# Optimization experiments

Hardware: AMD Instinct MI355X
Metric: run time of the kernel (lower is better)

## Reference

```python
import jax, jax.numpy as jnp
import numpy as np

N_VARS = 1_000_000
N_CLAUSES = 4_000_000
CLAUSE_SIZE = 3


def setup_inputs() -> dict:
    key = jax.random.key(0)
    k1, k2, k3 = jax.random.split(key, 3)
    assignment_logits = jax.random.normal(k1, (N_VARS,), dtype=jnp.float32)
    vars_in_clause = jax.random.randint(k2, (N_CLAUSES, CLAUSE_SIZE), 0, N_VARS, dtype=jnp.int64)
    signs = jax.random.randint(k3, (N_CLAUSES, CLAUSE_SIZE), 0, 2, dtype=jnp.int64)
    return {"assignment_logits": assignment_logits, "vars_in_clause": vars_in_clause, "signs": signs}


def reference(assignment_logits, vars_in_clause, signs):
    # assignments: [n_variables] in (0,1)
    assignments = jax.nn.sigmoid(assignment_logits)
    # gather literal values per clause: [n_clauses, clause_size]
    gathered = assignments[vars_in_clause]
    literal_values = jnp.where(signs == 1, gathered, 1.0 - gathered)
    # per-clause max (soft OR), then global min (hard AND)
    clause_satisfactions = literal_values.max(axis=1)  # [n_clauses]
    all_satisfied = clause_satisfactions.min()
    n_satisfied = (clause_satisfactions > 0.5).astype(jnp.float32).sum()
    return assignments, clause_satisfactions, all_satisfied, n_satisfied
```

## Files before the change

kernel.cpp:

```cpp
#include <hip/hip_runtime.h>
#include <math.h>

#define NV 1000000
#define NC 4000000
#define NGROUP (NC / 4)
#define G2 (NGROUP / 2)
#define TPB 1024
#define TPB_A 256

typedef _Float16 half_t;
typedef _Float16 half4_t __attribute__((ext_vector_type(4)));
typedef int   vint4   __attribute__((ext_vector_type(4)));
typedef float vfloat4 __attribute__((ext_vector_type(4)));

__device__ __forceinline__ float sigf(float x) { return 1.0f / (1.0f + __expf(-x)); }

__global__ __launch_bounds__(TPB_A) void tbl_build(
    const float* __restrict__ logits,
    half_t* __restrict__ tbl,
    float* __restrict__ out)
{
    const int i = blockIdx.x * TPB_A + threadIdx.x;
    if (i == 0) {
        out[NV + NC]     = INFINITY;
        out[NV + NC + 1] = 0.0f;
    }
    if (i < NV / 4) {
        vfloat4 v = ((const vfloat4*)logits)[i];
        half4_t h;
        h.x = (half_t)sigf(v.x); h.y = (half_t)sigf(v.y);
        h.z = (half_t)sigf(v.z); h.w = (half_t)sigf(v.w);
        ((half4_t*)tbl)[i] = h;
    }
}

__device__ __forceinline__ float litv(float sg, int s) { return s ? sg : 1.0f - sg; }

__global__ __launch_bounds__(TPB) void sat_clauses(
    const float*  __restrict__ logits,
    const half_t* __restrict__ tbl,
    const vint4*  __restrict__ vars4,
    const vint4*  __restrict__ signs4,
    float* __restrict__ out)
{
    const int g = blockIdx.x * TPB + threadIdx.x;
    float minv = INFINITY;
    float fcnt = 0.0f;

    if (g < NV / 4) {
        vfloat4 v = ((const vfloat4*)logits)[g];
        vfloat4 r;
        r.x = sigf(v.x); r.y = sigf(v.y); r.z = sigf(v.z); r.w = sigf(v.w);
        ((vfloat4*)out)[g] = r;
    }

    if (g < G2) {
        const int h = g + G2;
        vint4 a0 = vars4[3 * g], a1 = vars4[3 * g + 1], a2 = vars4[3 * g + 2];
        vint4 b0 = vars4[3 * h], b1 = vars4[3 * h + 1], b2 = vars4[3 * h + 2];

        float u0  = (float)tbl[a0.x], u1  = (float)tbl[a0.y], u2  = (float)tbl[a0.z];
        float u3  = (float)tbl[a0.w], u4  = (float)tbl[a1.x], u5  = (float)tbl[a1.y];
        float u6  = (float)tbl[a1.z], u7  = (float)tbl[a1.w], u8  = (float)tbl[a2.x];
        float u9  = (float)tbl[a2.y], u10 = (float)tbl[a2.z], u11 = (float)tbl[a2.w];
        float w0  = (float)tbl[b0.x], w1  = (float)tbl[b0.y], w2  = (float)tbl[b0.z];
        float w3  = (float)tbl[b0.w], w4  = (float)tbl[b1.x], w5  = (float)tbl[b1.y];
        float w6  = (float)tbl[b1.z], w7  = (float)tbl[b1.w], w8  = (float)tbl[b2.x];
        float w9  = (float)tbl[b2.y], w10 = (float)tbl[b2.z], w11 = (float)tbl[b2.w];

        vint4 sa0 = signs4[3 * g], sa1 = signs4[3 * g + 1], sa2 = signs4[3 * g + 2];
        vint4 sb0 = signs4[3 * h], sb1 = signs4[3 * h + 1], sb2 = signs4[3 * h + 2];

        vfloat4 r, q;
        r.x = fmaxf(fmaxf(litv(u0, sa0.x), litv(u1,  sa0.y)), litv(u2,  sa0.z));
        r.y = fmaxf(fmaxf(litv(u3, sa0.w), litv(u4,  sa1.x)), litv(u5,  sa1.y));
        r.z = fmaxf(fmaxf(litv(u6, sa1.z), litv(u7,  sa1.w)), litv(u8,  sa2.x));
        r.w = fmaxf(fmaxf(litv(u9, sa2.y), litv(u10, sa2.z)), litv(u11, sa2.w));
        q.x = fmaxf(fmaxf(litv(w0, sb0.x), litv(w1,  sb0.y)), litv(w2,  sb0.z));
        q.y = fmaxf(fmaxf(litv(w3, sb0.w), litv(w4,  sb1.x)), litv(w5,  sb1.y));
        q.z = fmaxf(fmaxf(litv(w6, sb1.z), litv(w7,  sb1.w)), litv(w8,  sb2.x));
        q.w = fmaxf(fmaxf(litv(w9, sb2.y), litv(w10, sb2.z)), litv(w11, sb2.w));

        __builtin_nontemporal_store(r, (vfloat4*)(out + NV) + g);
        __builtin_nontemporal_store(q, (vfloat4*)(out + NV) + h);

        minv = fminf(fminf(fminf(r.x, r.y), fminf(r.z, r.w)),
                     fminf(fminf(q.x, q.y), fminf(q.z, q.w)));
        fcnt = (float)((r.x > 0.5f) + (r.y > 0.5f) + (r.z > 0.5f) + (r.w > 0.5f) +
                       (q.x > 0.5f) + (q.y > 0.5f) + (q.z > 0.5f) + (q.w > 0.5f));
    }

    #pragma unroll
    for (int off = 32; off > 0; off >>= 1) {
        minv = fminf(minv, __shfl_down(minv, off));
        fcnt += __shfl_down(fcnt, off);
    }
    __shared__ float smin[TPB / 64];
    __shared__ float scnt[TPB / 64];
    const int wave = threadIdx.x >> 6, lane = threadIdx.x & 63;
    if (lane == 0) { smin[wave] = minv; scnt[wave] = fcnt; }
    __syncthreads();
    if (threadIdx.x == 0) {
        float m = smin[0], s = scnt[0];
        #pragma unroll
        for (int w = 1; w < TPB / 64; ++w) { m = fminf(m, smin[w]); s += scnt[w]; }
        atomicMin((unsigned int*)(out + NV + NC), __float_as_uint(m));
        atomicAdd(out + NV + NC + 1, s);
    }
}

extern "C" void kernel_launch(void* const* d_in, const int* in_sizes, int n_in,
                              void* d_out, int out_size, void* d_ws, size_t ws_size,
                              hipStream_t stream) {
    const float* logits = (const float*)d_in[0];
    const vint4* vars4  = (const vint4*)d_in[1];
    const vint4* signs4 = (const vint4*)d_in[2];
    float* out = (float*)d_out;
    half_t* tbl = (half_t*)d_ws;

    const int blkA = (NV / 4 + TPB_A - 1) / TPB_A;
    tbl_build<<<blkA, TPB_A, 0, stream>>>(logits, tbl, out);

    const int blkB = (G2 + TPB - 1) / TPB;
    sat_clauses<<<blkB, TPB, 0, stream>>>(logits, tbl, vars4, signs4, out);
}
```

Baseline: 73.59 us.

## Drop fp16 sigmoid table and gather raw fp32 logits with per-literal sigmoid

Removes the table-build kernel that precomputed fp16 sigmoids. The clause kernel now gathers fp32 logits directly and computes sigmoid(±x) for each literal. A trivial one-thread kernel seeds the min and count accumulators, and block size drops from 1024 to 256. This trades a full table-build pass for more gather bytes, since the gathered table is now 4 MB of fp32 instead of 2 MB of fp16, plus 24 extra exp evaluations per thread.

```diff
diff --git a/kernel.cpp b/kernel.cpp
--- a/kernel.cpp
+++ b/kernel.cpp
@@ -5,42 +5,24 @@
 #define NC 4000000
 #define NGROUP (NC / 4)
 #define G2 (NGROUP / 2)
-#define TPB 1024
-#define TPB_A 256
+#define TPB 256
 
-typedef _Float16 half_t;
-typedef _Float16 half4_t __attribute__((ext_vector_type(4)));
 typedef int   vint4   __attribute__((ext_vector_type(4)));
 typedef float vfloat4 __attribute__((ext_vector_type(4)));
 
 __device__ __forceinline__ float sigf(float x) { return 1.0f / (1.0f + __expf(-x)); }
 
-__global__ __launch_bounds__(TPB_A) void tbl_build(
-    const float* __restrict__ logits,
-    half_t* __restrict__ tbl,
-    float* __restrict__ out)
-{
-    const int i = blockIdx.x * TPB_A + threadIdx.x;
-    if (i == 0) {
-        out[NV + NC]     = INFINITY;
-        out[NV + NC + 1] = 0.0f;
-    }
-    if (i < NV / 4) {
-        vfloat4 v = ((const vfloat4*)logits)[i];
-        half4_t h;
-        h.x = (half_t)sigf(v.x); h.y = (half_t)sigf(v.y);
-        h.z = (half_t)sigf(v.z); h.w = (half_t)sigf(v.w);
-        ((half4_t*)tbl)[i] = h;
-    }
+__global__ void sat_seed(float* __restrict__ sc) {
+    sc[0] = INFINITY;
+    sc[1] = 0.0f;
 }
 
-__device__ __forceinline__ float litv(float sg, int s) { return s ? sg : 1.0f - sg; }
+__device__ __forceinline__ float litv(float x, int s) { return sigf(s ? x : -x); }
 
-__global__ __launch_bounds__(TPB) void sat_clauses(
-    const float*  __restrict__ logits,
-    const half_t* __restrict__ tbl,
-    const vint4*  __restrict__ vars4,
-    const vint4*  __restrict__ signs4,
+__global__ __launch_bounds__(TPB) void sat_fused(
+    const float* __restrict__ logits,
+    const vint4* __restrict__ vars4,
+    const vint4* __restrict__ signs4,
     float* __restrict__ out)
 {
     const int g = blockIdx.x * TPB + threadIdx.x;
@@ -59,14 +41,14 @@
         vint4 a0 = vars4[3 * g], a1 = vars4[3 * g + 1], a2 = vars4[3 * g + 2];
         vint4 b0 = vars4[3 * h], b1 = vars4[3 * h + 1], b2 = vars4[3 * h + 2];
 
-        float u0  = (float)tbl[a0.x], u1  = (float)tbl[a0.y], u2  = (float)tbl[a0.z];
-        float u3  = (float)tbl[a0.w], u4  = (float)tbl[a1.x], u5  = (float)tbl[a1.y];
-        float u6  = (float)tbl[a1.z], u7  = (float)tbl[a1.w], u8  = (float)tbl[a2.x];
-        float u9  = (float)tbl[a2.y], u10 = (float)tbl[a2.z], u11 = (float)tbl[a2.w];
-        float w0  = (float)tbl[b0.x], w1  = (float)tbl[b0.y], w2  = (float)tbl[b0.z];
-        float w3  = (float)tbl[b0.w], w4  = (float)tbl[b1.x], w5  = (float)tbl[b1.y];
-        float w6  = (float)tbl[b1.z], w7  = (float)tbl[b1.w], w8  = (float)tbl[b2.x];
-        float w9  = (float)tbl[b2.y], w10 = (float)tbl[b2.z], w11 = (float)tbl[b2.w];
+        float u0  = logits[a0.x], u1  = logits[a0.y], u2  = logits[a0.z];
+        float u3  = logits[a0.w], u4  = logits[a1.x], u5  = logits[a1.y];
+        float u6  = logits[a1.z], u7  = logits[a1.w], u8  = logits[a2.x];
+        float u9  = logits[a2.y], u10 = logits[a2.z], u11 = logits[a2.w];
+        float w0  = logits[b0.x], w1  = logits[b0.y], w2  = logits[b0.z];
+        float w3  = logits[b0.w], w4  = logits[b1.x], w5  = logits[b1.y];
+        float w6  = logits[b1.z], w7  = logits[b1.w], w8  = logits[b2.x];
+        float w9  = logits[b2.y], w10 = logits[b2.z], w11 = logits[b2.w];
 
         vint4 sa0 = signs4[3 * g], sa1 = signs4[3 * g + 1], sa2 = signs4[3 * g + 2];
         vint4 sb0 = signs4[3 * h], sb1 = signs4[3 * h + 1], sb2 = signs4[3 * h + 2];
@@ -116,11 +98,9 @@
     const vint4* vars4  = (const vint4*)d_in[1];
     const vint4* signs4 = (const vint4*)d_in[2];
     float* out = (float*)d_out;
-    half_t* tbl = (half_t*)d_ws;
 
-    const int blkA = (NV / 4 + TPB_A - 1) / TPB_A;
-    tbl_build<<<blkA, TPB_A, 0, stream>>>(logits, tbl, out);
+    sat_seed<<<1, 1, 0, stream>>>(out + NV + NC);
 
     const int blkB = (G2 + TPB - 1) / TPB;
-    sat_clauses<<<blkB, TPB, 0, stream>>>(logits, tbl, vars4, signs4, out);
+    sat_fused<<<blkB, TPB, 0, stream>>>(logits, vars4, signs4, out);
 }
```

New measurement: 92.71 us. 26.0% more time.
